# Kernel optimization log

Measured on AMD Instinct MI355X. Metric: run time of the kernel, lower is better.

Reference implementation:

```python
import jax, jax.numpy as jnp
import numpy as np

N, E = 25000, 400000
IN, HID, OUT = 128, 256, 128
T = 4                      # towers
F1, F2 = HID // T, OUT // T  # per-tower out dims (divide_input=False)
A = 12                     # len(aggregators)=4 * len(scalers)=3
EPS_STD = 1e-5
EPS_BN = 1e-5


def _glorot(k, shape):
    fin, fout = shape[-2], shape[-1]
    lim = float(np.sqrt(6.0 / (fin + fout)))
    return jax.random.uniform(k, shape, jnp.float32, -lim, lim)


def setup_inputs():
    key = jax.random.key(0)
    ks = jax.random.split(key, 10)
    x = jax.random.normal(ks[0], (N, IN), jnp.float32)
    edge_index = jax.random.randint(ks[1], (2, E), 0, N, dtype=jnp.int32)
    # avg_deg['log'] buffer of PNAConv: mean over nodes of log(deg+1)
    deg = jax.ops.segment_sum(jnp.ones((E,), jnp.float32), edge_index[1], num_segments=N)
    avg_log = jnp.mean(jnp.log(deg + 1.0)).astype(jnp.float32)
    return dict(
        x=x, edge_index=edge_index, avg_log=avg_log,
        pre1_W=_glorot(ks[2], (T, 2 * IN, F1)), pre1_b=jnp.zeros((T, F1), jnp.float32),
        post1_W=_glorot(ks[3], (T, IN + A * F1, F1)), post1_b=jnp.zeros((T, F1), jnp.float32),
        lin1_W=_glorot(ks[4], (T * F1, HID)), lin1_b=jnp.zeros((HID,), jnp.float32),
        bn1_g=jnp.ones((HID,), jnp.float32), bn1_b=jnp.zeros((HID,), jnp.float32),
        pre2_W=_glorot(ks[5], (T, 2 * HID, F2)), pre2_b=jnp.zeros((T, F2), jnp.float32),
        post2_W=_glorot(ks[6], (T, HID + A * F2, F2)), post2_b=jnp.zeros((T, F2), jnp.float32),
        lin2_W=_glorot(ks[7], (T * F2, OUT)), lin2_b=jnp.zeros((OUT,), jnp.float32),
        bn2_g=jnp.ones((OUT,), jnp.float32), bn2_b=jnp.zeros((OUT,), jnp.float32),
    )


def _pna(x, src, tgt, preW, preB, postW, postB, linW, linB, avg_log):
    """PNAConv: towers=T, divide_input=False, pre_layers=post_layers=1,
    aggregators [mean,min,max,std], scalers [identity,amplification,attenuation]."""
    n = x.shape[0]
    # message: per tower Linear on concat([x_i, x_j]) where i=target, j=source
    h = jnp.concatenate([x[tgt], x[src]], axis=-1)            # [E, 2*F_in]
    msg = jnp.einsum('ec,tcf->etf', h, preW) + preB           # [E, T, F]
    ones = jnp.ones((msg.shape[0],), msg.dtype)
    deg = jax.ops.segment_sum(ones, tgt, num_segments=n)      # in-degree [n]
    degc = jnp.maximum(deg, 1.0)[:, None, None]
    s1 = jax.ops.segment_sum(msg, tgt, num_segments=n)
    mean = s1 / degc
    s2 = jax.ops.segment_sum(msg * msg, tgt, num_segments=n)
    var = jnp.maximum(s2 / degc - mean * mean, 0.0)
    std = jnp.sqrt(var + EPS_STD)
    has = (deg > 0.0)[:, None, None]
    mn = jnp.where(has, jax.ops.segment_min(msg, tgt, num_segments=n), 0.0)
    mx = jnp.where(has, jax.ops.segment_max(msg, tgt, num_segments=n), 0.0)
    agg = jnp.concatenate([mean, mn, mx, std], axis=-1)       # [n, T, 4F]
    dlog = jnp.log(jnp.maximum(deg, 1.0) + 1.0)[:, None, None]
    out = jnp.concatenate([agg, agg * (dlog / avg_log), agg * (avg_log / dlog)], axis=-1)  # [n, T, 12F]
    xt = jnp.broadcast_to(x[:, None, :], (n, T, x.shape[-1]))
    post_in = jnp.concatenate([xt, out], axis=-1)             # [n, T, F_in + 12F]
    post = jnp.einsum('ntc,tcf->ntf', post_in, postW) + postB # [n, T, F]
    return post.reshape(n, -1) @ linW + linB                  # [n, out]


def _bn(x, g, b):
    # BatchNorm1d training-mode math: biased batch variance
    m = jnp.mean(x, axis=0)
    v = jnp.mean((x - m) ** 2, axis=0)
    return g * (x - m) / jnp.sqrt(v + EPS_BN) + b


def reference(x, edge_index, avg_log, pre1_W, pre1_b, post1_W, post1_b, lin1_W, lin1_b,
              bn1_g, bn1_b, pre2_W, pre2_b, post2_W, post2_b, lin2_W, lin2_b, bn2_g, bn2_b):
    src, tgt = edge_index[0], edge_index[1]
    h = _pna(x, src, tgt, pre1_W, pre1_b, post1_W, post1_b, lin1_W, lin1_b, avg_log)
    h = jax.nn.relu(_bn(jnp.nan_to_num(h), bn1_g, bn1_b))
    h = _pna(h, src, tgt, pre2_W, pre2_b, post2_W, post2_b, lin2_W, lin2_b, avg_log)
    h = jax.nn.relu(_bn(jnp.nan_to_num(h), bn2_g, bn2_b))
    return h
```

## Files before the change

### kernel.cpp

```cpp
#include <hip/hip_runtime.h>
#include <hip/hip_bf16.h>
#include <float.h>
#include <math.h>

typedef __hip_bfloat16 bf16;
typedef __attribute__((ext_vector_type(8))) short short8;
typedef __attribute__((ext_vector_type(4))) float f32x4;

__device__ __forceinline__ float bf2f(bf16 v){ return __bfloat162float(v); }
__device__ __forceinline__ void stv(float* p, float v){ *p = v; }
__device__ __forceinline__ void stv(bf16* p, float v){ *p = __float2bfloat16(v); }
__device__ __forceinline__ float nanfix(float v){
  if (v != v) return 0.f;
  return fminf(fmaxf(v, -FLT_MAX), FLT_MAX);
}
__device__ __forceinline__ unsigned short f2bu(float f){
  unsigned u = __float_as_uint(f);
  unsigned r = u + 0x7FFFu + ((u>>16)&1u);
  return (unsigned short)(r>>16);
}
template<int VEC>
__device__ __forceinline__ void ldbf(const bf16* p, float (&o)[VEC]){
  if constexpr (VEC==4){
    ushort4 r = *(const ushort4*)p;
    o[0]=__uint_as_float((unsigned)r.x<<16); o[1]=__uint_as_float((unsigned)r.y<<16);
    o[2]=__uint_as_float((unsigned)r.z<<16); o[3]=__uint_as_float((unsigned)r.w<<16);
  } else {
    ushort2 r = *(const ushort2*)p;
    o[0]=__uint_as_float((unsigned)r.x<<16); o[1]=__uint_as_float((unsigned)r.y<<16);
  }
}

__device__ __forceinline__ void gl_lds16(const bf16* g, bf16* l){
  __builtin_amdgcn_global_load_lds(
      (const __attribute__((address_space(1))) void*)g,
      (__attribute__((address_space(3))) void*)l, 16, 0, 0);
}

__global__ void k_scan1(const int* __restrict__ deg, int* __restrict__ bsum, int N){
  __shared__ int sm[256];
  int i = blockIdx.x*256 + threadIdx.x;
  sm[threadIdx.x] = (i < N) ? deg[i] : 0;
  __syncthreads();
  for (int off = 128; off > 0; off >>= 1){
    if (threadIdx.x < off) sm[threadIdx.x] += sm[threadIdx.x + off];
    __syncthreads();
  }
  if (threadIdx.x == 0) bsum[blockIdx.x] = sm[0];
}

__global__ void k_scan2(int* __restrict__ bsum, int NB){
  __shared__ int sm[1024];
  int tid = threadIdx.x;
  sm[tid] = (tid < NB) ? bsum[tid] : 0;
  __syncthreads();
  for (int off = 1; off < 1024; off <<= 1){
    int t = (tid >= off) ? sm[tid-off] : 0;
    __syncthreads();
    sm[tid] += t;
    __syncthreads();
  }
  if (tid < NB) bsum[tid] = (tid == 0) ? 0 : sm[tid-1];
}

__global__ void k_scan3(const int* __restrict__ deg, const int* __restrict__ bsum,
                        int* __restrict__ offs, int N){
  __shared__ int sm[256];
  int tid = threadIdx.x;
  int i = blockIdx.x*256 + tid;
  int v = (i < N) ? deg[i] : 0;
  sm[tid] = v; __syncthreads();
  for (int off = 1; off < 256; off <<= 1){
    int t = (tid >= off) ? sm[tid-off] : 0;
    __syncthreads();
    sm[tid] += t;
    __syncthreads();
  }
  if (i < N) offs[i+1] = bsum[blockIdx.x] + sm[tid];
  if (i == 0) offs[0] = 0;
}

__global__ void k_scatter(const int* __restrict__ src, const int* __restrict__ tgt,
                          const int* __restrict__ offs, int* __restrict__ cnt,
                          int* __restrict__ ssrc, int E){
  int e = blockIdx.x*blockDim.x + threadIdx.x;
  if (e < E){
    int t = tgt[e];
    int pos = offs[t] + atomicAdd(&cnt[t], 1);
    ssrc[pos] = src[e];
  }
}

__device__ __forceinline__ void rp_pqT(const float* preW, const float* preB,
                                       bf16* WpqT, float* bpq, int K, int F, int idx){
  int NC = 4*F;
  int total = 2*NC*K;
  if (idx < total){
    int j = idx/K, c = idx%K;
    int half = j/NC, jj = j%NC, t = jj/F, f = jj%F;
    WpqT[idx] = __float2bfloat16(preW[(t*2*K + half*K + c)*F + f]);
  }
  if (idx < 2*NC) bpq[idx] = (idx < NC) ? preB[idx] : 0.f;
}
__device__ __forceinline__ void rp_xT(const float* postW, const float* postB,
                                      bf16* WxT, float* bpost, int KX, int F, int idx){
  int NC = 4*F; int KP = KX + 12*F;
  if (idx < NC*KX){
    int j = idx/KX, c = idx%KX, t = j/F, f = j%F;
    WxT[idx] = __float2bfloat16(postW[(t*KP + c)*F + f]);
  }
  if (idx < NC) bpost[idx] = postB[idx];
}
__device__ __forceinline__ void rp_agg3(const float* postW, bf16* Wagg3,
                                        int KX, int F, int idx){
  int K4F = 4*F; int KP = KX + 12*F;
  int total = 4*3*F*K4F;
  if (idx < total){
    int k = idx % K4F; int r = idx / K4F;
    int zr = r % (3*F); int t = r / (3*F);
    int s = zr / F, f = zr % F;
    Wagg3[idx] = __float2bfloat16(postW[((size_t)(t*KP + KX + s*K4F + k))*F + f]);
  }
}
__device__ __forceinline__ void rp_linT(const float* linW, bf16* WlinT,
                                        int K, int NC, int idx){
  if (idx < NC*K){
    int j = idx/K, c = idx%K;
    WlinT[idx] = __float2bfloat16(linW[c*NC + j]);
  }
}

struct SetupArgs {
  const float *pre1W, *pre1b, *post1W, *post1b, *lin1W;
  const float *pre2W, *pre2b, *post2W, *post2b, *lin2W;
  const float *x;
  const int *tgt;
  bf16 *WpqT1, *WxT1, *Wagg31, *lin1WT;
  bf16 *WpqT2, *WxT2, *Wagg32, *lin2WT;
  bf16 *x_bf;
  int *deg;
  float *bpq1, *bpost1, *bpq2, *bpost2;
  int nx4;
  int E;
  int gstride;
};

__global__ void k_setup(SetupArgs a){
  int idx = blockIdx.x*256 + threadIdx.x;
  switch (blockIdx.y){
    case 0: rp_pqT (a.pre1W, a.pre1b, a.WpqT1, a.bpq1, 128, 64, idx); break;
    case 1: rp_xT  (a.post1W, a.post1b, a.WxT1, a.bpost1, 128, 64, idx); break;
    case 2: rp_agg3(a.post1W, a.Wagg31, 128, 64, idx); break;
    case 3: rp_linT(a.lin1W, a.lin1WT, 256, 256, idx); break;
    case 4: rp_pqT (a.pre2W, a.pre2b, a.WpqT2, a.bpq2, 256, 32, idx); break;
    case 5: rp_xT  (a.post2W, a.post2b, a.WxT2, a.bpost2, 256, 32, idx); break;
    case 6: rp_agg3(a.post2W, a.Wagg32, 256, 32, idx); break;
    case 7: rp_linT(a.lin2W, a.lin2WT, 128, 128, idx); break;
    case 8:
      for (int i = idx; i < a.nx4; i += a.gstride){
        float4 v = *(const float4*)(a.x + (size_t)i*4);
        ushort4 o = make_ushort4(f2bu(v.x), f2bu(v.y), f2bu(v.z), f2bu(v.w));
        *(ushort4*)(a.x_bf + (size_t)i*4) = o;
      }
      break;
    case 9:
      for (int e = idx; e < a.E; e += a.gstride)
        atomicAdd(&a.deg[a.tgt[e]], 1);
      break;
  }
}

template<typename TO, bool STATS>
__global__ __launch_bounds__(256) void k_mgemm(
    const bf16* __restrict__ A, int lda,
    const bf16* __restrict__ Bt,
    const float* __restrict__ bias,
    TO* __restrict__ Cout, int ldc,
    int N, int K, int NC, float* __restrict__ part)
{
  __shared__ __align__(16) bf16 As[2][64*32];
  __shared__ __align__(16) bf16 Bs[2][64*32];
  __shared__ float sstat[4][2][16][2];
  int n0 = blockIdx.y*64;
  int j0 = blockIdx.x*64;
  int tid = threadIdx.x;
  int srow = tid>>2, skoff = (tid&3)*8;
  int wave = tid>>6, lane = tid&63;
  int wy = (wave>>1)*32, wx = (wave&1)*32;
  int l15 = lane&15, q = lane>>4;
  f32x4 acc[2][2] = {};
  const bf16* Ag = A  + (size_t)(n0 + srow)*lda + skoff;
  const bf16* Bg = Bt + (size_t)(j0 + srow)*K   + skoff;
  int nt = K >> 5;
  gl_lds16(Ag, &As[0][tid*8]);
  gl_lds16(Bg, &Bs[0][tid*8]);
  __syncthreads();
  for (int t = 0; t < nt; t++){
    int cur = t & 1;
    if (t + 1 < nt){
      gl_lds16(Ag + (t+1)*32, &As[cur^1][tid*8]);
      gl_lds16(Bg + (t+1)*32, &Bs[cur^1][tid*8]);
    }
    short8 af[2], bfr[2];
    #pragma unroll
    for (int i = 0; i < 2; i++){
      af[i]  = *(const short8*)&As[cur][(wy + i*16 + l15)*32 + q*8];
      bfr[i] = *(const short8*)&Bs[cur][(wx + i*16 + l15)*32 + q*8];
    }
    #pragma unroll
    for (int mi = 0; mi < 2; mi++)
      #pragma unroll
      for (int ni = 0; ni < 2; ni++)
        acc[mi][ni] = __builtin_amdgcn_mfma_f32_16x16x32_bf16(af[mi], bfr[ni], acc[mi][ni], 0, 0, 0);
    __syncthreads();
  }
  float cs[2] = {0.f, 0.f}, cq[2] = {0.f, 0.f};
  #pragma unroll
  for (int mi = 0; mi < 2; mi++){
    #pragma unroll
    for (int ni = 0; ni < 2; ni++){
      #pragma unroll
      for (int r = 0; r < 4; r++){
        int n  = n0 + wy + mi*16 + q*4 + r;
        int jj = j0 + wx + ni*16 + l15;
        if (n < N && jj < NC){
          float v = acc[mi][ni][r] + bias[jj];
          stv(&Cout[(size_t)n*ldc + jj], v);
          if constexpr (STATS){ cs[ni] += v; cq[ni] = fmaf(v, v, cq[ni]); }
        }
      }
    }
  }
  if constexpr (STATS){
    #pragma unroll
    for (int ni = 0; ni < 2; ni++){
      float s = cs[ni], qq = cq[ni];
      s  += __shfl_xor(s, 16);  s  += __shfl_xor(s, 32);
      qq += __shfl_xor(qq, 16); qq += __shfl_xor(qq, 32);
      if (q == 0){ sstat[wave][ni][l15][0] = s; sstat[wave][ni][l15][1] = qq; }
    }
    __syncthreads();
    if (tid < 64){
      int j = tid;
      int wa = (j < 32) ? 0 : 1, wb = wa + 2;
      int ni = (j & 31) >> 4, li = j & 15;
      float s  = sstat[wa][ni][li][0] + sstat[wb][ni][li][0];
      float qq = sstat[wa][ni][li][1] + sstat[wb][ni][li][1];
      part[(size_t)blockIdx.y*2*ldc + (j0 + j)]       = s;
      part[(size_t)blockIdx.y*2*ldc + ldc + (j0 + j)] = qq;
    }
  }
}

template<int COLS>
__global__ __launch_bounds__(256) void k_postagg(
    const bf16* __restrict__ agg,
    const bf16* __restrict__ Wagg3,
    const bf16* __restrict__ PQX, int ldq, int cinOff,
    const float* __restrict__ scal,
    bf16* __restrict__ Cout, int ldc, int N)
{
  constexpr int K4F = 4*COLS;
  constexpr int ROWS3 = 3*COLS;
  constexpr int NI = COLS/32;
  constexpr int LDA_AGG = 16*COLS;
  __shared__ __align__(16) bf16 As[2][64*32];
  __shared__ __align__(16) bf16 Bs[2][ROWS3*32];
  int z = blockIdx.z;
  int n0 = blockIdx.y*64;
  int tid = threadIdx.x;
  int srow = tid>>2, skoff = (tid&3)*8;
  int wave = tid>>6, lane = tid&63;
  int wy = (wave>>1)*32;
  int wx = (wave&1)*(COLS/2);
  int l15 = lane&15, q = lane>>4;
  f32x4 acc[2][NI][3] = {};
  const bf16* Ag = agg + (size_t)z*K4F + (size_t)(n0 + srow)*LDA_AGG + skoff;
  const bf16* Bg = Wagg3 + (size_t)z*ROWS3*K4F + (size_t)srow*K4F + skoff;
  constexpr int NT = K4F/32;
  gl_lds16(Ag, &As[0][tid*8]);
  #pragma unroll
  for (int r = 0; r < ROWS3/64 + ((ROWS3%64)?1:0); r++){
    int rr = srow + r*64;
    if (rr < ROWS3) gl_lds16(Bg + (size_t)r*64*K4F, &Bs[0][rr*32 + skoff]);
  }
  __syncthreads();
  for (int t = 0; t < NT; t++){
    int cur = t & 1;
    if (t + 1 < NT){
      gl_lds16(Ag + (t+1)*32, &As[cur^1][tid*8]);
      #pragma unroll
      for (int r = 0; r < ROWS3/64 + ((ROWS3%64)?1:0); r++){
        int rr = srow + r*64;
        if (rr < ROWS3) gl_lds16(Bg + (size_t)r*64*K4F + (t+1)*32, &Bs[cur^1][rr*32 + skoff]);
      }
    }
    short8 af[2];
    #pragma unroll
    for (int i = 0; i < 2; i++)
      af[i] = *(const short8*)&As[cur][(wy + i*16 + l15)*32 + q*8];
    #pragma unroll
    for (int s = 0; s < 3; s++){
      #pragma unroll
      for (int ni = 0; ni < NI; ni++){
        short8 bfr = *(const short8*)&Bs[cur][(s*COLS + wx + ni*16 + l15)*32 + q*8];
        #pragma unroll
        for (int mi = 0; mi < 2; mi++)
          acc[mi][ni][s] = __builtin_amdgcn_mfma_f32_16x16x32_bf16(af[mi], bfr, acc[mi][ni][s], 0, 0, 0);
      }
    }
    __syncthreads();
  }
  #pragma unroll
  for (int mi = 0; mi < 2; mi++){
    #pragma unroll
    for (int ni = 0; ni < NI; ni++){
      int jj = wx + ni*16 + l15;
      int jg = z*COLS + jj;
      #pragma unroll
      for (int r = 0; r < 4; r++){
        int n = n0 + wy + mi*16 + q*4 + r;
        if (n < N){
          float s1 = scal[2*n], s2 = scal[2*n+1];
          float cin = bf2f(PQX[(size_t)n*ldq + cinOff + jg]);
          float v = cin + acc[mi][ni][0][r] + s1*acc[mi][ni][1][r] + s2*acc[mi][ni][2][r];
          Cout[(size_t)n*ldc + jg] = __float2bfloat16(v);
        }
      }
    }
  }
}

template<int NC, int F>
__global__ __launch_bounds__(256) void k_agg(const bf16* __restrict__ PQ, int lda,
    const int* __restrict__ ssrc, const int* __restrict__ offs,
    const float* __restrict__ avgp,
    bf16* __restrict__ agg, float* __restrict__ scal, int N){
  constexpr int VEC = NC/64;
  int wave = threadIdx.x>>6, lane = threadIdx.x&63;
  int n = blockIdx.x*4 + wave;
  if (n >= N) return;
  int c0 = lane*VEC;
  float p[VEC];
  ldbf<VEC>(PQ + (size_t)n*lda + c0, p);
  int s0 = offs[n], s1 = offs[n+1];
  float sum[VEC], sq[VEC], mn[VEC], mx[VEC];
  #pragma unroll
  for (int v=0;v<VEC;v++){ sum[v]=0.f; sq[v]=0.f; mn[v]=FLT_MAX; mx[v]=-FLT_MAX; }
  const bf16* Q = PQ + NC + c0;
  int i = s0;
  for (; i+7 < s1; i += 8){
    int se[8];
    #pragma unroll
    for (int u=0;u<8;u++) se[u] = ssrc[i+u];
    float qv[8][VEC];
    #pragma unroll
    for (int u=0;u<8;u++) ldbf<VEC>(Q + (size_t)se[u]*lda, qv[u]);
    #pragma unroll
    for (int u=0;u<8;u++){
      #pragma unroll
      for (int v=0;v<VEC;v++){
        float qq = qv[u][v];
        sum[v] += qq; sq[v] = fmaf(qq,qq,sq[v]);
        mn[v] = fminf(mn[v], qq); mx[v] = fmaxf(mx[v], qq);
      }
    }
  }
  for (; i+3 < s1; i += 4){
    int se[4];
    #pragma unroll
    for (int u=0;u<4;u++) se[u] = ssrc[i+u];
    float qv[4][VEC];
    #pragma unroll
    for (int u=0;u<4;u++) ldbf<VEC>(Q + (size_t)se[u]*lda, qv[u]);
    #pragma unroll
    for (int u=0;u<4;u++){
      #pragma unroll
      for (int v=0;v<VEC;v++){
        float qq = qv[u][v];
        sum[v] += qq; sq[v] = fmaf(qq,qq,sq[v]);
        mn[v] = fminf(mn[v], qq); mx[v] = fmaxf(mx[v], qq);
      }
    }
  }
  for (; i < s1; i++){
    int sa = ssrc[i];
    float qa[VEC];
    ldbf<VEC>(Q + (size_t)sa*lda, qa);
    #pragma unroll
    for (int v=0;v<VEC;v++){
      float qq = qa[v];
      sum[v]+=qq; sq[v]=fmaf(qq,qq,sq[v]); mn[v]=fminf(mn[v],qq); mx[v]=fmaxf(mx[v],qq);
    }
  }
  int deg = s1-s0;
  float degf = (float)deg;
  float degc = fmaxf(degf, 1.f);
  unsigned short um[VEC], un[VEC], ux[VEC], us[VEC];
  #pragma unroll
  for (int v=0;v<VEC;v++){
    float pv = p[v];
    float sum_m = fmaf(degf, pv, sum[v]);
    float sq_m  = sq[v] + 2.f*pv*sum[v] + degf*pv*pv;
    float mean = sum_m/degc;
    float var = fmaxf(sq_m/degc - mean*mean, 0.f);
    float sd = sqrtf(var + 1e-5f);
    float mnv = deg>0 ? pv + mn[v] : 0.f;
    float mxv = deg>0 ? pv + mx[v] : 0.f;
    um[v]=f2bu(mean); un[v]=f2bu(mnv); ux[v]=f2bu(mxv); us[v]=f2bu(sd);
  }
  int t = c0 / F, f0 = c0 % F;
  bf16* base = agg + (size_t)n*4*NC + (size_t)t*4*F + f0;
  if constexpr (VEC==4){
    *(ushort4*)(base)       = make_ushort4(um[0],um[1],um[2],um[3]);
    *(ushort4*)(base + F)   = make_ushort4(un[0],un[1],un[2],un[3]);
    *(ushort4*)(base + 2*F) = make_ushort4(ux[0],ux[1],ux[2],ux[3]);
    *(ushort4*)(base + 3*F) = make_ushort4(us[0],us[1],us[2],us[3]);
  } else {
    *(ushort2*)(base)       = make_ushort2(um[0],um[1]);
    *(ushort2*)(base + F)   = make_ushort2(un[0],un[1]);
    *(ushort2*)(base + 2*F) = make_ushort2(ux[0],ux[1]);
    *(ushort2*)(base + 3*F) = make_ushort2(us[0],us[1]);
  }
  if (lane==0){
    float dlog = logf(degc + 1.f);
    float avg = *avgp;
    scal[2*n]   = dlog/avg;
    scal[2*n+1] = avg/dlog;
  }
}

template<int C>
__global__ __launch_bounds__(256) void k_bn_final(const float* __restrict__ part, int PB,
                                                  float* __restrict__ stats){
  int c = blockIdx.x*256 + threadIdx.x;
  if (c >= 2*C) return;
  int CH = gridDim.y;
  int per = (PB + CH - 1)/CH;
  int p0 = blockIdx.y*per, p1 = min(p0 + per, PB);
  float acc = 0.f;
  int p = p0;
  for (; p+4 <= p1; p += 4){
    acc += part[(size_t)p*2*C + c] + part[(size_t)(p+1)*2*C + c]
         + part[(size_t)(p+2)*2*C + c] + part[(size_t)(p+3)*2*C + c];
  }
  for (; p < p1; p++) acc += part[(size_t)p*2*C + c];
  atomicAdd(&stats[c], acc);
}

template<typename TO, int C>
__global__ void k_bn_apply(const bf16* __restrict__ h, const float* __restrict__ stats,
     const float* __restrict__ g, const float* __restrict__ b,
     TO* __restrict__ out, int N){
  int idx = blockIdx.x*blockDim.x + threadIdx.x;
  if (idx >= N*(C/4)) return;
  int c = (idx % (C/4))*4;
  float fn = (float)N;
  float v[4];
  ldbf<4>(h + (size_t)idx*4, v);
  float r[4];
  #pragma unroll
  for (int k = 0; k < 4; k++){
    float m = stats[c+k]/fn;
    float var = fmaxf(stats[C+c+k]/fn - m*m, 0.f);
    float inv = rsqrtf(var + 1e-5f);
    float vv = nanfix(v[k]);
    r[k] = fmaxf(g[c+k]*(vv - m)*inv + b[c+k], 0.f);
  }
  if constexpr (sizeof(TO) == 4){
    float4 o = {r[0], r[1], r[2], r[3]};
    *(float4*)((float*)out + (size_t)idx*4) = o;
  } else {
    ushort4 o = make_ushort4(f2bu(r[0]), f2bu(r[1]), f2bu(r[2]), f2bu(r[3]));
    *(ushort4*)((bf16*)out + (size_t)idx*4) = o;
  }
}

static inline int cdiv(int a, int b){ return (a + b - 1)/b; }

extern "C" void kernel_launch(void* const* d_in, const int* in_sizes, int n_in,
                              void* d_out, int out_size, void* d_ws, size_t ws_size,
                              hipStream_t stream){
  const int IN = 128, HID = 256, T = 4, F1 = 64, F2 = 32;
  const int N = in_sizes[0]/IN;
  const int E = in_sizes[1]/2;
  const int NC1 = T*F1;
  const int NC2 = T*F2;
  const int LDQ1 = 2*NC1 + NC1;
  const int LDQ2 = 2*NC2 + NC2;

  const float* x      = (const float*)d_in[0];
  const int*   ei     = (const int*)  d_in[1];
  const int*   srcE   = ei;
  const int*   tgtE   = ei + E;
  const float* avgp   = (const float*)d_in[2];
  const float* pre1W  = (const float*)d_in[3];
  const float* pre1b  = (const float*)d_in[4];
  const float* post1W = (const float*)d_in[5];
  const float* post1b = (const float*)d_in[6];
  const float* lin1W  = (const float*)d_in[7];
  const float* lin1b  = (const float*)d_in[8];
  const float* bn1g   = (const float*)d_in[9];
  const float* bn1b   = (const float*)d_in[10];
  const float* pre2W  = (const float*)d_in[11];
  const float* pre2b  = (const float*)d_in[12];
  const float* post2W = (const float*)d_in[13];
  const float* post2b = (const float*)d_in[14];
  const float* lin2W  = (const float*)d_in[15];
  const float* lin2b  = (const float*)d_in[16];
  const float* bn2g   = (const float*)d_in[17];
  const float* bn2b   = (const float*)d_in[18];

  char* w = (char*)d_ws;
  auto alloc = [&](size_t bytes)->void*{
    void* p = (void*)w; w += (bytes + 255) & ~(size_t)255; return p;
  };
  bf16* BT1    = (bf16*)alloc((size_t)LDQ1*IN*2);
  bf16* WpqT1  = BT1;              bf16* WxT1 = BT1 + (size_t)2*NC1*IN;
  float* bias1 = (float*)alloc((size_t)LDQ1*4);
  float* bpq1  = bias1;            float* bpost1 = bias1 + 2*NC1;
  bf16* Wagg31 = (bf16*)alloc((size_t)T*3*F1*4*F1*2);
  bf16* lin1WT = (bf16*)alloc((size_t)HID*NC1*2);
  bf16* BT2    = (bf16*)alloc((size_t)LDQ2*HID*2);
  bf16* WpqT2  = BT2;              bf16* WxT2 = BT2 + (size_t)2*NC2*HID;
  float* bias2 = (float*)alloc((size_t)LDQ2*4);
  float* bpq2  = bias2;            float* bpost2 = bias2 + 2*NC2;
  bf16* Wagg32 = (bf16*)alloc((size_t)T*3*F2*4*F2*2);
  bf16* lin2WT = (bf16*)alloc((size_t)128*NC2*2);
  int* deg_i   = (int*)alloc((size_t)N*4);
  int* cnt     = (int*)alloc((size_t)N*4);
  float* stats = (float*)alloc(1024*4);
  size_t zbytes = (size_t)((char*)stats - (char*)deg_i) + 1024*4;
  int* offs    = (int*)alloc((size_t)(N+1)*4);
  int* bsum    = (int*)alloc((size_t)cdiv(N,256)*4);
  int* ssrc    = (int*)alloc((size_t)E*4);
  bf16* x_bf   = (bf16*)alloc((size_t)N*IN*2);
  bf16* PQX    = (bf16*)alloc((size_t)N*LDQ1*2);
  bf16* aggb   = (bf16*)alloc((size_t)N*4*NC1*2);
  float* scal  = (float*)alloc((size_t)N*2*4);
  bf16* postbb = (bf16*)alloc((size_t)N*256*2);
  bf16* hpre   = (bf16*)alloc((size_t)N*256*2);
  bf16* h1b    = (bf16*)alloc((size_t)N*256*2);
  int NB = cdiv(N,64);
  float* part  = (float*)alloc((size_t)NB*512*4);

  hipMemsetAsync(deg_i, 0, zbytes, stream);

  int sgx = cdiv(T*3*F1*4*F1, 256);
  SetupArgs sa = { pre1W, pre1b, post1W, post1b, lin1W,
                   pre2W, pre2b, post2W, post2b, lin2W,
                   x, tgtE,
                   WpqT1, WxT1, Wagg31, lin1WT,
                   WpqT2, WxT2, Wagg32, lin2WT,
                   x_bf, deg_i,
                   bpq1, bpost1, bpq2, bpost2,
                   N*IN/4, E, sgx*256 };
  k_setup<<<dim3(sgx, 10),256,0,stream>>>(sa);

  int NBs = cdiv(N,256);
  k_scan1<<<NBs,256,0,stream>>>(deg_i, bsum, N);
  k_scan2<<<1,1024,0,stream>>>(bsum, NBs);
  k_scan3<<<NBs,256,0,stream>>>(deg_i, bsum, offs, N);
  k_scatter<<<cdiv(E,256),256,0,stream>>>(srcE, tgtE, offs, cnt, ssrc, E);

  k_mgemm<bf16,false><<<dim3(LDQ1/64,NB),256,0,stream>>>(x_bf, IN, BT1, bias1, PQX, LDQ1, N, IN, LDQ1, nullptr);
  k_agg<256,64><<<cdiv(N,4),256,0,stream>>>(PQX, LDQ1, ssrc, offs, avgp, aggb, scal, N);
  k_postagg<64><<<dim3(1,NB,T),256,0,stream>>>(aggb, Wagg31, PQX, LDQ1, 2*NC1, scal,
                                               postbb, NC1, N);
  k_mgemm<bf16,true><<<dim3(4,NB),256,0,stream>>>(postbb, NC1, lin1WT, lin1b, hpre, HID, N, NC1, HID, part);
  k_bn_final<256><<<dim3(2,4),256,0,stream>>>(part, NB, stats);
  k_bn_apply<bf16,256><<<cdiv(N*64,256),256,0,stream>>>(hpre, stats, bn1g, bn1b, h1b, N);

  k_mgemm<bf16,false><<<dim3(LDQ2/64,NB),256,0,stream>>>(h1b, HID, BT2, bias2, PQX, LDQ2, N, HID, LDQ2, nullptr);
  k_agg<128,32><<<cdiv(N,4),256,0,stream>>>(PQX, LDQ2, ssrc, offs, avgp, aggb, scal, N);
  k_postagg<32><<<dim3(1,NB,T),256,0,stream>>>(aggb, Wagg32, PQX, LDQ2, 2*NC2, scal,
                                               postbb, NC2, N);
  k_mgemm<bf16,true><<<dim3(2,NB),256,0,stream>>>(postbb, NC2, lin2WT, lin2b, hpre, 128, N, NC2, 128, part);
  k_bn_final<128><<<dim3(1,4),256,0,stream>>>(part, NB, stats + 512);
  k_bn_apply<float,128><<<cdiv(N*32,256),256,0,stream>>>(hpre, stats + 512, bn2g, bn2b, (float*)d_out, N);
}
```

Measured before the change: 359.4 us.

## Split each aggregation wave across two edges with wider gathers and shuffled indices

The neighbor aggregation kernel now has each half-wave handle a different edge. Each lane loads 8 or 4 bf16 values per gather instead of 4 or 2, so two source rows are in flight per load instruction. Edge indices are loaded cooperatively once per group of 8 and broadcast with shuffles, with the next group prefetched. The two half-wave partial statistics are combined with xor-shuffles at the end. The row stride becomes a compile-time template parameter and the division by degree becomes a reciprocal multiply. This adds shuffle overhead and masked tail handling for odd edge counts.

```diff
diff --git a/kernel.cpp b/kernel.cpp
--- a/kernel.cpp
+++ b/kernel.cpp
@@ -331,98 +331,145 @@
   }
 }
 
-template<int NC, int F>
-__global__ __launch_bounds__(256) void k_agg(const bf16* __restrict__ PQ, int lda,
+template<int NC, int F, int LDA>
+__global__ __launch_bounds__(256) void k_agg(const bf16* __restrict__ PQ,
     const int* __restrict__ ssrc, const int* __restrict__ offs,
     const float* __restrict__ avgp,
-    bf16* __restrict__ agg, float* __restrict__ scal, int N){
-  constexpr int VEC = NC/64;
-  int wave = threadIdx.x>>6, lane = threadIdx.x&63;
-  int n = blockIdx.x*4 + wave;
+    bf16* __restrict__ agg, float* __restrict__ scal, int N)
+{
+  constexpr int VEC = NC/32;
+  constexpr int VU  = VEC/2;
+  int lane = threadIdx.x & 63;
+  int n = __builtin_amdgcn_readfirstlane((int)(blockIdx.x*4 + (threadIdx.x>>6)));
   if (n >= N) return;
-  int c0 = lane*VEC;
+  int lsub = lane & 31, esub = lane >> 5;
+  int c0 = lsub * VEC;
   float p[VEC];
-  ldbf<VEC>(PQ + (size_t)n*lda + c0, p);
+  {
+    unsigned pr[VU];
+    const unsigned* ps = (const unsigned*)(PQ + (size_t)n*LDA + c0);
+    if constexpr (VU==4){ uint4 t = *(const uint4*)ps; pr[0]=t.x; pr[1]=t.y; pr[2]=t.z; pr[3]=t.w; }
+    else                { uint2 t = *(const uint2*)ps; pr[0]=t.x; pr[1]=t.y; }
+    #pragma unroll
+    for (int k=0;k<VU;k++){
+      p[2*k]   = __uint_as_float(pr[k]<<16);
+      p[2*k+1] = __uint_as_float(pr[k]&0xffff0000u);
+    }
+  }
   int s0 = offs[n], s1 = offs[n+1];
+  int deg = s1 - s0;
   float sum[VEC], sq[VEC], mn[VEC], mx[VEC];
   #pragma unroll
   for (int v=0;v<VEC;v++){ sum[v]=0.f; sq[v]=0.f; mn[v]=FLT_MAX; mx[v]=-FLT_MAX; }
-  const bf16* Q = PQ + NC + c0;
-  int i = s0;
-  for (; i+7 < s1; i += 8){
-    int se[8];
-    #pragma unroll
-    for (int u=0;u<8;u++) se[u] = ssrc[i+u];
-    float qv[8][VEC];
-    #pragma unroll
-    for (int u=0;u<8;u++) ldbf<VEC>(Q + (size_t)se[u]*lda, qv[u]);
-    #pragma unroll
-    for (int u=0;u<8;u++){
-      #pragma unroll
-      for (int v=0;v<VEC;v++){
-        float qq = qv[u][v];
-        sum[v] += qq; sq[v] = fmaf(qq,qq,sq[v]);
-        mn[v] = fminf(mn[v], qq); mx[v] = fmaxf(mx[v], qq);
-      }
-    }
-  }
-  for (; i+3 < s1; i += 4){
-    int se[4];
-    #pragma unroll
-    for (int u=0;u<4;u++) se[u] = ssrc[i+u];
-    float qv[4][VEC];
-    #pragma unroll
-    for (int u=0;u<4;u++) ldbf<VEC>(Q + (size_t)se[u]*lda, qv[u]);
-    #pragma unroll
-    for (int u=0;u<4;u++){
-      #pragma unroll
-      for (int v=0;v<VEC;v++){
-        float qq = qv[u][v];
-        sum[v] += qq; sq[v] = fmaf(qq,qq,sq[v]);
-        mn[v] = fminf(mn[v], qq); mx[v] = fmaxf(mx[v], qq);
-      }
-    }
-  }
-  for (; i < s1; i++){
-    int sa = ssrc[i];
-    float qa[VEC];
-    ldbf<VEC>(Q + (size_t)sa*lda, qa);
-    #pragma unroll
-    for (int v=0;v<VEC;v++){
-      float qq = qa[v];
-      sum[v]+=qq; sq[v]=fmaf(qq,qq,sq[v]); mn[v]=fminf(mn[v],qq); mx[v]=fmaxf(mx[v],qq);
-    }
-  }
-  int deg = s1-s0;
+  const char* Qc = (const char*)(PQ + NC);
+  unsigned coffB = (unsigned)(c0*2);
+  if (deg > 0){
+    int last = s1 - 1;
+    int raw = ssrc[min(s0 + (lane&7), last)];
+    int e8 = deg & ~7;
+    for (int ii = 0; ii < e8; ii += 8){
+      int rawn = ssrc[min(s0 + ii + 8 + (lane&7), last)];
+      unsigned ro[4][VU];
+      #pragma unroll
+      for (int s=0;s<4;s++){
+        int se = __shfl(raw, s*2 + esub);
+        unsigned off = (unsigned)se*(unsigned)(LDA*2) + coffB;
+        if constexpr (VU==4){
+          uint4 t = *(const uint4*)(Qc + off);
+          ro[s][0]=t.x; ro[s][1]=t.y; ro[s][2]=t.z; ro[s][3]=t.w;
+        } else {
+          uint2 t = *(const uint2*)(Qc + off);
+          ro[s][0]=t.x; ro[s][1]=t.y;
+        }
+      }
+      #pragma unroll
+      for (int s=0;s<4;s++){
+        #pragma unroll
+        for (int k=0;k<VU;k++){
+          float q0 = __uint_as_float(ro[s][k]<<16);
+          float q1 = __uint_as_float(ro[s][k]&0xffff0000u);
+          sum[2*k]   += q0; sq[2*k]   = fmaf(q0,q0,sq[2*k]);
+          mn[2*k]    = fminf(mn[2*k],q0);  mx[2*k]   = fmaxf(mx[2*k],q0);
+          sum[2*k+1] += q1; sq[2*k+1] = fmaf(q1,q1,sq[2*k+1]);
+          mn[2*k+1]  = fminf(mn[2*k+1],q1); mx[2*k+1] = fmaxf(mx[2*k+1],q1);
+        }
+      }
+      raw = rawn;
+    }
+    int i = s0 + e8;
+    if (i < s1){
+      #pragma unroll
+      for (int s=0;s<4;s++){
+        if (i + s*2 < s1){
+          int ei = i + s*2 + esub;
+          int se = __shfl(raw, s*2 + esub);
+          unsigned off = (unsigned)se*(unsigned)(LDA*2) + coffB;
+          unsigned r2[VU];
+          if constexpr (VU==4){
+            uint4 t = *(const uint4*)(Qc + off);
+            r2[0]=t.x; r2[1]=t.y; r2[2]=t.z; r2[3]=t.w;
+          } else {
+            uint2 t = *(const uint2*)(Qc + off);
+            r2[0]=t.x; r2[1]=t.y;
+          }
+          bool valid = ei < s1;
+          #pragma unroll
+          for (int k=0;k<VU;k++){
+            float q0 = __uint_as_float(r2[k]<<16);
+            float q1 = __uint_as_float(r2[k]&0xffff0000u);
+            float t0 = valid ? q0 : 0.f;
+            float t1 = valid ? q1 : 0.f;
+            sum[2*k]   += t0; sq[2*k]   = fmaf(t0,q0,sq[2*k]);
+            mn[2*k]    = fminf(mn[2*k],q0);  mx[2*k]   = fmaxf(mx[2*k],q0);
+            sum[2*k+1] += t1; sq[2*k+1] = fmaf(t1,q1,sq[2*k+1]);
+            mn[2*k+1]  = fminf(mn[2*k+1],q1); mx[2*k+1] = fmaxf(mx[2*k+1],q1);
+          }
+        }
+      }
+    }
+  }
+  #pragma unroll
+  for (int v=0;v<VEC;v++){
+    sum[v] += __shfl_xor(sum[v], 32);
+    sq[v]  += __shfl_xor(sq[v], 32);
+    mn[v]   = fminf(mn[v], __shfl_xor(mn[v], 32));
+    mx[v]   = fmaxf(mx[v], __shfl_xor(mx[v], 32));
+  }
   float degf = (float)deg;
   float degc = fmaxf(degf, 1.f);
+  float rdeg = 1.f/degc;
   unsigned short um[VEC], un[VEC], ux[VEC], us[VEC];
   #pragma unroll
   for (int v=0;v<VEC;v++){
     float pv = p[v];
     float sum_m = fmaf(degf, pv, sum[v]);
     float sq_m  = sq[v] + 2.f*pv*sum[v] + degf*pv*pv;
-    float mean = sum_m/degc;
-    float var = fmaxf(sq_m/degc - mean*mean, 0.f);
+    float mean = sum_m*rdeg;
+    float var = fmaxf(fmaf(sq_m, rdeg, -mean*mean), 0.f);
     float sd = sqrtf(var + 1e-5f);
     float mnv = deg>0 ? pv + mn[v] : 0.f;
     float mxv = deg>0 ? pv + mx[v] : 0.f;
     um[v]=f2bu(mean); un[v]=f2bu(mnv); ux[v]=f2bu(mxv); us[v]=f2bu(sd);
   }
-  int t = c0 / F, f0 = c0 % F;
-  bf16* base = agg + (size_t)n*4*NC + (size_t)t*4*F + f0;
-  if constexpr (VEC==4){
-    *(ushort4*)(base)       = make_ushort4(um[0],um[1],um[2],um[3]);
-    *(ushort4*)(base + F)   = make_ushort4(un[0],un[1],un[2],un[3]);
-    *(ushort4*)(base + 2*F) = make_ushort4(ux[0],ux[1],ux[2],ux[3]);
-    *(ushort4*)(base + 3*F) = make_ushort4(us[0],us[1],us[2],us[3]);
-  } else {
-    *(ushort2*)(base)       = make_ushort2(um[0],um[1]);
-    *(ushort2*)(base + F)   = make_ushort2(un[0],un[1]);
-    *(ushort2*)(base + 2*F) = make_ushort2(ux[0],ux[1]);
-    *(ushort2*)(base + 3*F) = make_ushort2(us[0],us[1]);
-  }
-  if (lane==0){
+  if (esub == 0){
+    int t = c0 / F, f0 = c0 % F;
+    bf16* base = agg + (size_t)n*(4*NC) + (size_t)t*(4*F) + f0;
+    if constexpr (VEC==8){
+      short8 o0, o1, o2, o3;
+      #pragma unroll
+      for (int v=0;v<8;v++){ o0[v]=(short)um[v]; o1[v]=(short)un[v]; o2[v]=(short)ux[v]; o3[v]=(short)us[v]; }
+      *(short8*)(base)       = o0;
+      *(short8*)(base + F)   = o1;
+      *(short8*)(base + 2*F) = o2;
+      *(short8*)(base + 3*F) = o3;
+    } else {
+      *(ushort4*)(base)       = make_ushort4(um[0],um[1],um[2],um[3]);
+      *(ushort4*)(base + F)   = make_ushort4(un[0],un[1],un[2],un[3]);
+      *(ushort4*)(base + 2*F) = make_ushort4(ux[0],ux[1],ux[2],ux[3]);
+      *(ushort4*)(base + 3*F) = make_ushort4(us[0],us[1],us[2],us[3]);
+    }
+  }
+  if (lane == 0){
     float dlog = logf(degc + 1.f);
     float avg = *avgp;
     scal[2*n]   = dlog/avg;
@@ -564,7 +611,7 @@
   k_scatter<<<cdiv(E,256),256,0,stream>>>(srcE, tgtE, offs, cnt, ssrc, E);
 
   k_mgemm<bf16,false><<<dim3(LDQ1/64,NB),256,0,stream>>>(x_bf, IN, BT1, bias1, PQX, LDQ1, N, IN, LDQ1, nullptr);
-  k_agg<256,64><<<cdiv(N,4),256,0,stream>>>(PQX, LDQ1, ssrc, offs, avgp, aggb, scal, N);
+  k_agg<256,64,768><<<cdiv(N,4),256,0,stream>>>(PQX, ssrc, offs, avgp, aggb, scal, N);
   k_postagg<64><<<dim3(1,NB,T),256,0,stream>>>(aggb, Wagg31, PQX, LDQ1, 2*NC1, scal,
                                                postbb, NC1, N);
   k_mgemm<bf16,true><<<dim3(4,NB),256,0,stream>>>(postbb, NC1, lin1WT, lin1b, hpre, HID, N, NC1, HID, part);
@@ -572,7 +619,7 @@
   k_bn_apply<bf16,256><<<cdiv(N*64,256),256,0,stream>>>(hpre, stats, bn1g, bn1b, h1b, N);
 
   k_mgemm<bf16,false><<<dim3(LDQ2/64,NB),256,0,stream>>>(h1b, HID, BT2, bias2, PQX, LDQ2, N, HID, LDQ2, nullptr);
-  k_agg<128,32><<<cdiv(N,4),256,0,stream>>>(PQX, LDQ2, ssrc, offs, avgp, aggb, scal, N);
+  k_agg<128,32,384><<<cdiv(N,4),256,0,stream>>>(PQX, ssrc, offs, avgp, aggb, scal, N);
   k_postagg<32><<<dim3(1,NB,T),256,0,stream>>>(aggb, Wagg32, PQX, LDQ2, 2*NC2, scal,
                                                postbb, NC2, N);
   k_mgemm<bf16,true><<<dim3(2,NB),256,0,stream>>>(postbb, NC2, lin2WT, lin2b, hpre, 128, N, NC2, 128, part);
```

New measurement: 367.5 us. 1.02x slower.

## Enlarge postagg row tile to 128 and software-pipeline neighbor index loads in agg

Applied to the files above, without the earlier changes.

The post-aggregation GEMM now handles 128 node rows per block instead of 64, so each wave computes 4 MFMA row fragments and every B-weight tile is reused across twice as many rows. The aggregation kernel compiles the leading dimension in, keeps node and edge offsets in scalar registers, and fetches the next 8 source indices while the current 8 rows are gathered. Tails are handled by clamping indices and masking the sums, which replaces the separate 4-wide and scalar remainder loops. In exchange, the postagg kernel uses more registers and LDS and launches fewer blocks, which could lower occupancy.

```diff
diff --git a/kernel.cpp b/kernel.cpp
--- a/kernel.cpp
+++ b/kernel.cpp
@@ -264,40 +264,45 @@
   constexpr int ROWS3 = 3*COLS;
   constexpr int NI = COLS/32;
   constexpr int LDA_AGG = 16*COLS;
-  __shared__ __align__(16) bf16 As[2][64*32];
+  constexpr int BROW3 = (ROWS3 + 63)/64;
+  __shared__ __align__(16) bf16 As[2][128*32];
   __shared__ __align__(16) bf16 Bs[2][ROWS3*32];
   int z = blockIdx.z;
-  int n0 = blockIdx.y*64;
+  int n0 = blockIdx.y*128;
   int tid = threadIdx.x;
   int srow = tid>>2, skoff = (tid&3)*8;
   int wave = tid>>6, lane = tid&63;
-  int wy = (wave>>1)*32;
+  int wy = (wave>>1)*64;
   int wx = (wave&1)*(COLS/2);
   int l15 = lane&15, q = lane>>4;
-  f32x4 acc[2][NI][3] = {};
+  f32x4 acc[4][NI][3] = {};
   const bf16* Ag = agg + (size_t)z*K4F + (size_t)(n0 + srow)*LDA_AGG + skoff;
   const bf16* Bg = Wagg3 + (size_t)z*ROWS3*K4F + (size_t)srow*K4F + skoff;
   constexpr int NT = K4F/32;
-  gl_lds16(Ag, &As[0][tid*8]);
+  gl_lds16(Ag,                          &As[0][srow*32 + skoff]);
+  gl_lds16(Ag + (size_t)64*LDA_AGG,     &As[0][(srow+64)*32 + skoff]);
   #pragma unroll
-  for (int r = 0; r < ROWS3/64 + ((ROWS3%64)?1:0); r++){
+  for (int r = 0; r < BROW3; r++){
     int rr = srow + r*64;
-    if (rr < ROWS3) gl_lds16(Bg + (size_t)r*64*K4F, &Bs[0][rr*32 + skoff]);
+    if (ROWS3 % 64 == 0 || rr < ROWS3)
+      gl_lds16(Bg + (size_t)r*64*K4F, &Bs[0][rr*32 + skoff]);
   }
   __syncthreads();
   for (int t = 0; t < NT; t++){
     int cur = t & 1;
     if (t + 1 < NT){
-      gl_lds16(Ag + (t+1)*32, &As[cur^1][tid*8]);
+      gl_lds16(Ag + (t+1)*32,                      &As[cur^1][srow*32 + skoff]);
+      gl_lds16(Ag + (t+1)*32 + (size_t)64*LDA_AGG, &As[cur^1][(srow+64)*32 + skoff]);
       #pragma unroll
-      for (int r = 0; r < ROWS3/64 + ((ROWS3%64)?1:0); r++){
+      for (int r = 0; r < BROW3; r++){
         int rr = srow + r*64;
-        if (rr < ROWS3) gl_lds16(Bg + (size_t)r*64*K4F + (t+1)*32, &Bs[cur^1][rr*32 + skoff]);
-      }
-    }
-    short8 af[2];
-    #pragma unroll
-    for (int i = 0; i < 2; i++)
+        if (ROWS3 % 64 == 0 || rr < ROWS3)
+          gl_lds16(Bg + (size_t)r*64*K4F + (t+1)*32, &Bs[cur^1][rr*32 + skoff]);
+      }
+    }
+    short8 af[4];
+    #pragma unroll
+    for (int i = 0; i < 4; i++)
       af[i] = *(const short8*)&As[cur][(wy + i*16 + l15)*32 + q*8];
     #pragma unroll
     for (int s = 0; s < 3; s++){
@@ -305,14 +310,14 @@
       for (int ni = 0; ni < NI; ni++){
         short8 bfr = *(const short8*)&Bs[cur][(s*COLS + wx + ni*16 + l15)*32 + q*8];
         #pragma unroll
-        for (int mi = 0; mi < 2; mi++)
+        for (int mi = 0; mi < 4; mi++)
           acc[mi][ni][s] = __builtin_amdgcn_mfma_f32_16x16x32_bf16(af[mi], bfr, acc[mi][ni][s], 0, 0, 0);
       }
     }
     __syncthreads();
   }
   #pragma unroll
-  for (int mi = 0; mi < 2; mi++){
+  for (int mi = 0; mi < 4; mi++){
     #pragma unroll
     for (int ni = 0; ni < NI; ni++){
       int jj = wx + ni*16 + l15;
@@ -331,79 +336,82 @@
   }
 }
 
-template<int NC, int F>
-__global__ __launch_bounds__(256) void k_agg(const bf16* __restrict__ PQ, int lda,
+template<int NC, int F, int LDA>
+__global__ __launch_bounds__(256) void k_agg(const bf16* __restrict__ PQ,
     const int* __restrict__ ssrc, const int* __restrict__ offs,
     const float* __restrict__ avgp,
-    bf16* __restrict__ agg, float* __restrict__ scal, int N){
+    bf16* __restrict__ agg, float* __restrict__ scal, int N)
+{
   constexpr int VEC = NC/64;
-  int wave = threadIdx.x>>6, lane = threadIdx.x&63;
-  int n = blockIdx.x*4 + wave;
+  int lane = threadIdx.x & 63;
+  int n = __builtin_amdgcn_readfirstlane((int)(blockIdx.x*4 + (threadIdx.x>>6)));
   if (n >= N) return;
   int c0 = lane*VEC;
   float p[VEC];
-  ldbf<VEC>(PQ + (size_t)n*lda + c0, p);
-  int s0 = offs[n], s1 = offs[n+1];
+  ldbf<VEC>(PQ + (size_t)n*LDA + c0, p);
+  int s0 = __builtin_amdgcn_readfirstlane(offs[n]);
+  int s1 = __builtin_amdgcn_readfirstlane(offs[n+1]);
+  int deg = s1 - s0;
   float sum[VEC], sq[VEC], mn[VEC], mx[VEC];
   #pragma unroll
   for (int v=0;v<VEC;v++){ sum[v]=0.f; sq[v]=0.f; mn[v]=FLT_MAX; mx[v]=-FLT_MAX; }
   const bf16* Q = PQ + NC + c0;
-  int i = s0;
-  for (; i+7 < s1; i += 8){
+  if (deg > 0){
+    int last = s1 - 1;
     int se[8];
     #pragma unroll
-    for (int u=0;u<8;u++) se[u] = ssrc[i+u];
-    float qv[8][VEC];
-    #pragma unroll
-    for (int u=0;u<8;u++) ldbf<VEC>(Q + (size_t)se[u]*lda, qv[u]);
-    #pragma unroll
-    for (int u=0;u<8;u++){
+    for (int u=0;u<8;u++) se[u] = ssrc[min(s0+u, last)];
+    for (int i = s0; i < s1; i += 8){
+      int sn[8];
+      bool more = (i + 8 < s1);
+      if (more){
+        #pragma unroll
+        for (int u=0;u<8;u++) sn[u] = ssrc[min(i+8+u, last)];
+      }
+      float qv[8][VEC];
       #pragma unroll
-      for (int v=0;v<VEC;v++){
-        float qq = qv[u][v];
-        sum[v] += qq; sq[v] = fmaf(qq,qq,sq[v]);
-        mn[v] = fminf(mn[v], qq); mx[v] = fmaxf(mx[v], qq);
-      }
-    }
-  }
-  for (; i+3 < s1; i += 4){
-    int se[4];
-    #pragma unroll
-    for (int u=0;u<4;u++) se[u] = ssrc[i+u];
-    float qv[4][VEC];
-    #pragma unroll
-    for (int u=0;u<4;u++) ldbf<VEC>(Q + (size_t)se[u]*lda, qv[u]);
-    #pragma unroll
-    for (int u=0;u<4;u++){
-      #pragma unroll
-      for (int v=0;v<VEC;v++){
-        float qq = qv[u][v];
-        sum[v] += qq; sq[v] = fmaf(qq,qq,sq[v]);
-        mn[v] = fminf(mn[v], qq); mx[v] = fmaxf(mx[v], qq);
-      }
-    }
-  }
-  for (; i < s1; i++){
-    int sa = ssrc[i];
-    float qa[VEC];
-    ldbf<VEC>(Q + (size_t)sa*lda, qa);
-    #pragma unroll
-    for (int v=0;v<VEC;v++){
-      float qq = qa[v];
-      sum[v]+=qq; sq[v]=fmaf(qq,qq,sq[v]); mn[v]=fminf(mn[v],qq); mx[v]=fmaxf(mx[v],qq);
-    }
-  }
-  int deg = s1-s0;
+      for (int u=0;u<8;u++) ldbf<VEC>(Q + (size_t)se[u]*LDA, qv[u]);
+      int rem = s1 - i;
+      if (rem >= 8){
+        #pragma unroll
+        for (int u=0;u<8;u++){
+          #pragma unroll
+          for (int v=0;v<VEC;v++){
+            float qq = qv[u][v];
+            sum[v] += qq; sq[v] = fmaf(qq,qq,sq[v]);
+            mn[v] = fminf(mn[v],qq); mx[v] = fmaxf(mx[v],qq);
+          }
+        }
+      } else {
+        #pragma unroll
+        for (int u=0;u<8;u++){
+          bool valid = u < rem;
+          #pragma unroll
+          for (int v=0;v<VEC;v++){
+            float qq = qv[u][v];
+            float tq = valid ? qq : 0.f;
+            sum[v] += tq; sq[v] = fmaf(tq,qq,sq[v]);
+            mn[v] = fminf(mn[v],qq); mx[v] = fmaxf(mx[v],qq);
+          }
+        }
+      }
+      if (more){
+        #pragma unroll
+        for (int u=0;u<8;u++) se[u] = sn[u];
+      }
+    }
+  }
   float degf = (float)deg;
   float degc = fmaxf(degf, 1.f);
+  float rdeg = 1.f/degc;
   unsigned short um[VEC], un[VEC], ux[VEC], us[VEC];
   #pragma unroll
   for (int v=0;v<VEC;v++){
     float pv = p[v];
     float sum_m = fmaf(degf, pv, sum[v]);
     float sq_m  = sq[v] + 2.f*pv*sum[v] + degf*pv*pv;
-    float mean = sum_m/degc;
-    float var = fmaxf(sq_m/degc - mean*mean, 0.f);
+    float mean = sum_m*rdeg;
+    float var = fmaxf(fmaf(sq_m, rdeg, -mean*mean), 0.f);
     float sd = sqrtf(var + 1e-5f);
     float mnv = deg>0 ? pv + mn[v] : 0.f;
     float mxv = deg>0 ? pv + mx[v] : 0.f;
@@ -422,7 +430,7 @@
     *(ushort2*)(base + 2*F) = make_ushort2(ux[0],ux[1]);
     *(ushort2*)(base + 3*F) = make_ushort2(us[0],us[1]);
   }
-  if (lane==0){
+  if (lane == 0){
     float dlog = logf(degc + 1.f);
     float avg = *avgp;
     scal[2*n]   = dlog/avg;
@@ -542,6 +550,7 @@
   bf16* hpre   = (bf16*)alloc((size_t)N*256*2);
   bf16* h1b    = (bf16*)alloc((size_t)N*256*2);
   int NB = cdiv(N,64);
+  int NB128 = cdiv(N,128);
   float* part  = (float*)alloc((size_t)NB*512*4);
 
   hipMemsetAsync(deg_i, 0, zbytes, stream);
@@ -564,17 +573,17 @@
   k_scatter<<<cdiv(E,256),256,0,stream>>>(srcE, tgtE, offs, cnt, ssrc, E);
 
   k_mgemm<bf16,false><<<dim3(LDQ1/64,NB),256,0,stream>>>(x_bf, IN, BT1, bias1, PQX, LDQ1, N, IN, LDQ1, nullptr);
-  k_agg<256,64><<<cdiv(N,4),256,0,stream>>>(PQX, LDQ1, ssrc, offs, avgp, aggb, scal, N);
-  k_postagg<64><<<dim3(1,NB,T),256,0,stream>>>(aggb, Wagg31, PQX, LDQ1, 2*NC1, scal,
-                                               postbb, NC1, N);
+  k_agg<256,64,768><<<cdiv(N,4),256,0,stream>>>(PQX, ssrc, offs, avgp, aggb, scal, N);
+  k_postagg<64><<<dim3(1,NB128,T),256,0,stream>>>(aggb, Wagg31, PQX, LDQ1, 2*NC1, scal,
+                                                  postbb, NC1, N);
   k_mgemm<bf16,true><<<dim3(4,NB),256,0,stream>>>(postbb, NC1, lin1WT, lin1b, hpre, HID, N, NC1, HID, part);
   k_bn_final<256><<<dim3(2,4),256,0,stream>>>(part, NB, stats);
   k_bn_apply<bf16,256><<<cdiv(N*64,256),256,0,stream>>>(hpre, stats, bn1g, bn1b, h1b, N);
 
   k_mgemm<bf16,false><<<dim3(LDQ2/64,NB),256,0,stream>>>(h1b, HID, BT2, bias2, PQX, LDQ2, N, HID, LDQ2, nullptr);
-  k_agg<128,32><<<cdiv(N,4),256,0,stream>>>(PQX, LDQ2, ssrc, offs, avgp, aggb, scal, N);
-  k_postagg<32><<<dim3(1,NB,T),256,0,stream>>>(aggb, Wagg32, PQX, LDQ2, 2*NC2, scal,
-                                               postbb, NC2, N);
+  k_agg<128,32,384><<<cdiv(N,4),256,0,stream>>>(PQX, ssrc, offs, avgp, aggb, scal, N);
+  k_postagg<32><<<dim3(1,NB128,T),256,0,stream>>>(aggb, Wagg32, PQX, LDQ2, 2*NC2, scal,
+                                                  postbb, NC2, N);
   k_mgemm<bf16,true><<<dim3(2,NB),256,0,stream>>>(postbb, NC2, lin2WT, lin2b, hpre, 128, N, NC2, 128, part);
   k_bn_final<128><<<dim3(1,4),256,0,stream>>>(part, NB, stats + 512);
   k_bn_apply<float,128><<<cdiv(N*32,256),256,0,stream>>>(hpre, stats + 512, bn2g, bn2b, (float*)d_out, N);
```

New measurement: 364.2 us. About the same (+1.3%).
